# Kernel tuning notes

Measured on AMD Instinct MI355X. Metric: run time of the kernel, lower is better.

Reference implementation:

```python
import jax, jax.numpy as jnp
import numpy as np
from jax import lax

B, C, T = 8, 512, 2048
TEMP = 0.07
EPS = 1e-12


def setup_inputs() -> dict:
    key = jax.random.key(0)
    k1, k2, k3, k4 = jax.random.split(key, 4)
    x = jax.random.normal(k1, (B, C, T), dtype=jnp.float32)
    w_qkv = jax.random.normal(k2, (3 * C, C, 1), dtype=jnp.float32) * (1.0 / np.sqrt(C))
    w_dw = jax.random.normal(k3, (3 * C, 1, 3), dtype=jnp.float32) * (1.0 / np.sqrt(3))
    w_proj = jax.random.normal(k4, (C, C, 1), dtype=jnp.float32) * (1.0 / np.sqrt(C))
    return {"x": x, "w_qkv": w_qkv, "w_dw": w_dw, "w_proj": w_proj}


def _l2norm_ch(a):
    # F.normalize(a, dim=1): divide by L2 norm over channel dim, clamped at eps
    n = jnp.sqrt(jnp.sum(a * a, axis=1, keepdims=True))
    return a / jnp.maximum(n, EPS)


def reference(x, w_qkv, w_dw, w_proj):
    # 1x1 conv: [B,C,T] x [3C,C] -> [B,3C,T]
    qkv = jnp.einsum('bct,oc->bot', x, w_qkv[:, :, 0])
    # depthwise conv, kernel 3, padding 1, groups = 3C
    qkv = lax.conv_general_dilated(
        qkv, w_dw, window_strides=(1,), padding=[(1, 1)],
        dimension_numbers=('NCH', 'OIH', 'NCH'), feature_group_count=3 * C)
    q, k, v = jnp.split(qkv, 3, axis=1)  # each [B,C,T]
    q = _l2norm_ch(q)
    k = _l2norm_ch(k)
    # attn over tokens: [B,T,T]
    attn = jax.nn.softmax(jnp.einsum('bct,bcs->bts', q, k) / TEMP, axis=-1)
    out = jnp.einsum('bts,bcs->bct', attn, v)  # [B,C,T]
    return jnp.einsum('bct,oc->bot', out, w_proj[:, :, 0])
```

## Files before the change

### kernel.cpp

```cpp
#include <hip/hip_runtime.h>
#include <math.h>

static constexpr int B_ = 8, C_ = 512, T_ = 2048, C3_ = 1536;
static constexpr float INV_TEMP = 1.0f / 0.07f;

typedef __attribute__((ext_vector_type(8))) short short8;
typedef __attribute__((ext_vector_type(4))) float floatx4;

__device__ __forceinline__ float b2f(unsigned short u) {
  union { unsigned int i; float f; } v; v.i = ((unsigned int)u) << 16; return v.f;
}
__device__ __forceinline__ unsigned short f2b(float f) {
  union { float f; unsigned int i; } v; v.f = f;
  const unsigned int x = v.i;
  return (unsigned short)((x + 0x7FFFu + ((x >> 16) & 1u)) >> 16);
}
__device__ __forceinline__ void gld16(const unsigned short* g, unsigned short* l) {
  __builtin_amdgcn_global_load_lds(
      (const __attribute__((address_space(1))) void*)g,
      (__attribute__((address_space(3))) void*)l, 16, 0, 0);
}

template<int TM, bool OUT_BF16, int MODE>
__global__ __launch_bounds__(256)
void gemm_tn(const unsigned short* __restrict__ A, const unsigned short* __restrict__ B,
             void* __restrict__ Cout, int K, int lda, int ldb, int ldc,
             long long sA, long long sB, long long sC,
             const float* __restrict__ rs, const float* __restrict__ cs,
             float* __restrict__ denom, int rcStride, float scale)
{
  constexpr int NFA = TM / 64 * 2;

  const int bz = blockIdx.z;
  A += (long long)bz * sA;
  B += (long long)bz * sB;
  if (MODE == 2) { rs += (long long)bz * rcStride; cs += (long long)bz * rcStride;
                   denom += (long long)bz * rcStride; }
  if (MODE == 3) { rs += (long long)bz * rcStride; }
  const int m0 = blockIdx.y * TM, n0 = blockIdx.x * 128;
  const int tid = threadIdx.x;
  const int w = tid >> 6, lane = tid & 63;
  const int wm = (w >> 1) * (TM / 2), wn = (w & 1) * 64;
  const int rl = lane & 15, qd = lane >> 4;

  __shared__ __align__(16) unsigned short As[2][TM * 32];
  __shared__ __align__(16) unsigned short Bs[2][128 * 32];

  const int sr = lane >> 2, sg = lane & 3;
  const int aml0 = (TM == 128 ? 32 * w : 16 * w) + sr, aml1 = aml0 + 16;
  const int aq0 = sg ^ ((aml0 >> 1) & 3), aq1 = sg ^ ((aml1 >> 1) & 3);
  const unsigned short* gA0 = A + (long long)(m0 + aml0) * lda + aq0 * 8;
  const unsigned short* gA1 = A + (long long)(m0 + aml1) * lda + aq1 * 8;
  const int bml0 = 32 * w + sr, bml1 = bml0 + 16;
  const int bq0 = sg ^ ((bml0 >> 1) & 3), bq1 = sg ^ ((bml1 >> 1) & 3);
  const unsigned short* gB0 = B + (long long)(n0 + bml0) * ldb + bq0 * 8;
  const unsigned short* gB1 = B + (long long)(n0 + bml1) * ldb + bq1 * 8;

  int aoff[NFA], boff[4];
  #pragma unroll
  for (int i = 0; i < NFA; ++i) {
    const int mr = wm + i * 16 + rl;
    aoff[i] = mr * 32 + ((qd ^ ((mr >> 1) & 3)) * 8);
  }
  #pragma unroll
  for (int j = 0; j < 4; ++j) {
    const int nr = wn + j * 16 + rl;
    boff[j] = nr * 32 + ((qd ^ ((nr >> 1) & 3)) * 8);
  }

  floatx4 acc[NFA][4];
  #pragma unroll
  for (int i = 0; i < NFA; ++i)
    #pragma unroll
    for (int j = 0; j < 4; ++j) acc[i][j] = 0.0f;

  auto stage = [&](int t, int bf) {
    const int ko = t * 32;
    gld16(gA0 + ko, As[bf] + (TM == 128 ? 32 * w : 16 * w) * 32);
    if (TM == 128) gld16(gA1 + ko, As[bf] + (32 * w + 16) * 32);
    gld16(gB0 + ko, Bs[bf] + (32 * w) * 32);
    gld16(gB1 + ko, Bs[bf] + (32 * w + 16) * 32);
  };

  const int niter = K >> 5;
  stage(0, 0);
  for (int i = 0; i < niter; ++i) {
    const int buf = i & 1;
    __syncthreads();
    short8 fa[NFA], fb[4];
    #pragma unroll
    for (int ii = 0; ii < NFA; ++ii) fa[ii] = *(const short8*)(As[buf] + aoff[ii]);
    #pragma unroll
    for (int j = 0; j < 4; ++j) fb[j] = *(const short8*)(Bs[buf] + boff[j]);
    if (i + 1 < niter) stage(i + 1, buf ^ 1);
    #pragma unroll
    for (int ii = 0; ii < NFA; ++ii)
      #pragma unroll
      for (int j = 0; j < 4; ++j)
        acc[ii][j] = __builtin_amdgcn_mfma_f32_16x16x32_bf16(fa[ii], fb[j], acc[ii][j], 0, 0, 0);
  }

  #pragma unroll
  for (int i = 0; i < NFA; ++i) {
    #pragma unroll
    for (int r = 0; r < 4; ++r) {
      const int row = m0 + wm + i * 16 + qd * 4 + r;
      float rowf = 0.f;
      if (MODE == 2) rowf = rs[row] * scale;
      if (MODE == 3) rowf = 1.0f / rs[row];
      float rsum = 0.f;
      #pragma unroll
      for (int j = 0; j < 4; ++j) {
        const int col = n0 + wn + j * 16 + rl;
        float v = acc[i][j][r];
        if (MODE == 2) {
          const float s = v * rowf * cs[col];
          const unsigned short pb = f2b(__expf(s - scale));
          rsum += b2f(pb);
          ((unsigned short*)Cout)[(long long)bz * sC + (long long)row * ldc + col] = pb;
          continue;
        }
        if (MODE == 3) v *= rowf;
        const long long idx = (long long)bz * sC + (long long)row * ldc + col;
        if (OUT_BF16) ((unsigned short*)Cout)[idx] = f2b(v);
        else          ((float*)Cout)[idx] = v;
      }
      if (MODE == 2) {
        #pragma unroll
        for (int m = 1; m < 16; m <<= 1) rsum += __shfl_xor(rsum, m);
        if (rl == 0) atomicAdd(denom + row, rsum);
      }
    }
  }
}

__global__ __launch_bounds__(256)
void zero_f(float* __restrict__ p, int n)
{
  const int i = blockIdx.x * 256 + threadIdx.x;
  if (i < n) p[i] = 0.f;
}

__global__ __launch_bounds__(256)
void conv_xT(const float* __restrict__ x, unsigned short* __restrict__ xT)
{
  const int b = blockIdx.z, t0 = blockIdx.x * 32, c0 = blockIdx.y * 32;
  const int tx = threadIdx.x & 31, ty = threadIdx.x >> 5;
  __shared__ float tile[32][33];
  const float* src = x + (long long)b * C_ * T_;
  #pragma unroll
  for (int r = 0; r < 4; ++r)
    tile[ty + 8 * r][tx] = src[(long long)(c0 + ty + 8 * r) * T_ + t0 + tx];
  __syncthreads();
  unsigned short* dst = xT + (long long)b * T_ * C_;
  #pragma unroll
  for (int r = 0; r < 4; ++r)
    dst[(long long)(t0 + ty + 8 * r) * C_ + c0 + tx] = f2b(tile[tx][ty + 8 * r]);
}

__global__ __launch_bounds__(256)
void conv_bf(const float* __restrict__ in, unsigned short* __restrict__ out, int n)
{
  const int i = blockIdx.x * 256 + threadIdx.x;
  if (i < n) out[i] = f2b(in[i]);
}

__global__ __launch_bounds__(256)
void dw_v(const unsigned short* __restrict__ qkv, const float* __restrict__ wdw,
          unsigned short* __restrict__ vout)
{
  const long long idx = (long long)blockIdx.x * 256 + threadIdx.x;
  const int t = (int)(idx % T_);
  const long long rem = idx / T_;
  const int c = (int)(rem % C_), b = (int)(rem / C_);
  const unsigned short* src = qkv + ((long long)(b * C3_ + 2 * C_ + c)) * T_;
  const float* wp = wdw + (2 * C_ + c) * 3;
  const float xm = (t > 0)      ? b2f(src[t - 1]) : 0.f;
  const float x0 = b2f(src[t]);
  const float xp = (t < T_ - 1) ? b2f(src[t + 1]) : 0.f;
  vout[(long long)(b * C_ + c) * T_ + t] = f2b(fmaf(wp[0], xm, fmaf(wp[1], x0, wp[2] * xp)));
}

__global__ __launch_bounds__(256)
void dw_qk_t(const unsigned short* __restrict__ qkv, const float* __restrict__ wdw,
             unsigned short* __restrict__ qT, unsigned short* __restrict__ kT)
{
  const int bz = blockIdx.z, b = bz >> 1, p = bz & 1;
  const int t0 = blockIdx.x * 32, c0 = blockIdx.y * 32;
  const int tx = threadIdx.x & 31, ty = threadIdx.x >> 5;
  __shared__ float tin[32][34];
  __shared__ float tout[32][33];
  const int chb = b * C3_ + p * C_;
  #pragma unroll
  for (int r = 0; r < 4; ++r) {
    const int cy = ty + 8 * r;
    const unsigned short* src = qkv + (long long)(chb + c0 + cy) * T_;
    int t = t0 - 1 + tx;
    tin[cy][tx] = (t >= 0 && t < T_) ? b2f(src[t]) : 0.f;
    if (tx < 2) {
      const int t2 = t0 + 31 + tx;
      tin[cy][32 + tx] = (t2 < T_) ? b2f(src[t2]) : 0.f;
    }
  }
  __syncthreads();
  #pragma unroll
  for (int r = 0; r < 4; ++r) {
    const int cy = ty + 8 * r;
    const float* wp = wdw + (long long)(p * C_ + c0 + cy) * 3;
    tout[tx][cy] = fmaf(wp[0], tin[cy][tx], fmaf(wp[1], tin[cy][tx + 1], wp[2] * tin[cy][tx + 2]));
  }
  __syncthreads();
  unsigned short* dst = (p == 0 ? qT : kT) + (long long)b * T_ * C_;
  #pragma unroll
  for (int r = 0; r < 4; ++r)
    dst[(long long)(t0 + ty + 8 * r) * C_ + c0 + tx] = f2b(tout[ty + 8 * r][tx]);
}

__global__ __launch_bounds__(256)
void norms_k(const unsigned short* __restrict__ qT, const unsigned short* __restrict__ kT,
             float* __restrict__ inv_nq, float* __restrict__ inv_nk)
{
  const int wave = threadIdx.x >> 6, lane = threadIdx.x & 63;
  const long long row = (long long)blockIdx.x * 4 + wave;
  const unsigned short* src = (blockIdx.y == 0 ? qT : kT) + row * C_ + lane * 8;
  const uint4 u = *(const uint4*)src;
  float ss = 0.f;
  const unsigned int uu[4] = {u.x, u.y, u.z, u.w};
  #pragma unroll
  for (int i = 0; i < 4; ++i) {
    const float lo = b2f(uu[i] & 0xFFFF), hi = b2f(uu[i] >> 16);
    ss = fmaf(lo, lo, ss); ss = fmaf(hi, hi, ss);
  }
  #pragma unroll
  for (int m = 32; m; m >>= 1) ss += __shfl_xor(ss, m);
  if (lane == 0)
    (blockIdx.y == 0 ? inv_nq : inv_nk)[row] = 1.f / fmaxf(sqrtf(ss), 1e-12f);
}

extern "C" void kernel_launch(void* const* d_in, const int* in_sizes, int n_in,
                              void* d_out, int out_size, void* d_ws, size_t ws_size,
                              hipStream_t stream)
{
  const float* x      = (const float*)d_in[0];
  const float* w_qkv  = (const float*)d_in[1];
  const float* w_dw   = (const float*)d_in[2];
  const float* w_proj = (const float*)d_in[3];
  float* out = (float*)d_out;

  char* base = (char*)d_ws;
  unsigned short* xT      = (unsigned short*)base;
  unsigned short* wqkv_bf = (unsigned short*)(base + 16777216);
  unsigned short* av_t    = (unsigned short*)base;
  char* p = base + 67108864;
  unsigned short* qT = (unsigned short*)p; p += 16777216;
  unsigned short* kT = (unsigned short*)p; p += 16777216;
  unsigned short* vb = (unsigned short*)p; p += 16777216;
  unsigned short* attn   = (unsigned short*)p;
  unsigned short* qkv_bf = (unsigned short*)p;
  p += 67108864;
  unsigned short* wproj_bf = (unsigned short*)p; p += 524288;
  float* inv_nq = (float*)p; p += 65536;
  float* inv_nk = (float*)p; p += 65536;
  float* denom  = (float*)p;

  const long long TC = (long long)T_ * C_, TT = (long long)T_ * T_;

  conv_xT<<<dim3(T_ / 32, C_ / 32, B_), 256, 0, stream>>>(x, xT);
  conv_bf<<<(C3_ * C_) / 256, 256, 0, stream>>>(w_qkv, wqkv_bf, C3_ * C_);
  conv_bf<<<(C_ * C_) / 256, 256, 0, stream>>>(w_proj, wproj_bf, C_ * C_);
  zero_f<<<(B_ * T_) / 256, 256, 0, stream>>>(denom, B_ * T_);

  gemm_tn<128, true, 0><<<dim3(16, 12, B_), 256, 0, stream>>>(
      wqkv_bf, xT, qkv_bf, C_, C_, C_, T_,
      0LL, TC, (long long)C3_ * T_, nullptr, nullptr, nullptr, 0, 1.f);

  dw_v<<<(int)(((long long)B_ * C_ * T_) / 256), 256, 0, stream>>>(qkv_bf, w_dw, vb);
  dw_qk_t<<<dim3(T_ / 32, C_ / 32, B_ * 2), 256, 0, stream>>>(qkv_bf, w_dw, qT, kT);

  norms_k<<<dim3((B_ * T_) / 4, 2), 256, 0, stream>>>(qT, kT, inv_nq, inv_nk);

  gemm_tn<128, true, 2><<<dim3(16, 16, B_), 256, 0, stream>>>(
      qT, kT, attn, C_, C_, C_, T_,
      TC, TC, TT, inv_nq, inv_nk, denom, T_, INV_TEMP);

  gemm_tn<64, true, 3><<<dim3(4, 32, B_), 256, 0, stream>>>(
      attn, vb, av_t, T_, T_, T_, C_,
      TT, (long long)C_ * T_, TC, denom, nullptr, nullptr, T_, 1.f);

  gemm_tn<64, false, 0><<<dim3(16, 8, B_), 256, 0, stream>>>(
      wproj_bf, av_t, out, C_, C_, C_, T_,
      0LL, TC, (long long)C_ * T_, nullptr, nullptr, nullptr, 0, 1.f);
}
```

Baseline: 343.6 us.

## Replace direct global-to-LDS loads with register-staged double-buffered prefetch in GEMM

The GEMM main loop stops using global_load_lds and instead loads tiles into registers two iterations ahead, writes them into swizzled LDS double buffers, and syncs with an explicit lgkmcnt wait plus barrier. The aim is to hide global memory latency behind the MFMA work and to use wider per-thread 32-byte loads. The denominator zeroing moves into the norms kernel, which removes one kernel launch. The cost is higher register pressure from the staging registers, and the unrolled-by-two loop assumes an even iteration count.

```diff
diff --git a/kernel.cpp b/kernel.cpp
--- a/kernel.cpp
+++ b/kernel.cpp
@@ -15,11 +15,8 @@
   const unsigned int x = v.i;
   return (unsigned short)((x + 0x7FFFu + ((x >> 16) & 1u)) >> 16);
 }
-__device__ __forceinline__ void gld16(const unsigned short* g, unsigned short* l) {
-  __builtin_amdgcn_global_load_lds(
-      (const __attribute__((address_space(1))) void*)g,
-      (__attribute__((address_space(3))) void*)l, 16, 0, 0);
-}
+
+#define LGKM_BARRIER() asm volatile("s_waitcnt lgkmcnt(0)\n\ts_barrier" ::: "memory")
 
 template<int TM, bool OUT_BF16, int MODE>
 __global__ __launch_bounds__(256)
@@ -30,6 +27,7 @@
              float* __restrict__ denom, int rcStride, float scale)
 {
   constexpr int NFA = TM / 64 * 2;
+  constexpr int LA  = TM / 64;
 
   const int bz = blockIdx.z;
   A += (long long)bz * sA;
@@ -43,18 +41,26 @@
   const int wm = (w >> 1) * (TM / 2), wn = (w & 1) * 64;
   const int rl = lane & 15, qd = lane >> 4;
 
-  __shared__ __align__(16) unsigned short As[2][TM * 32];
-  __shared__ __align__(16) unsigned short Bs[2][128 * 32];
-
-  const int sr = lane >> 2, sg = lane & 3;
-  const int aml0 = (TM == 128 ? 32 * w : 16 * w) + sr, aml1 = aml0 + 16;
-  const int aq0 = sg ^ ((aml0 >> 1) & 3), aq1 = sg ^ ((aml1 >> 1) & 3);
-  const unsigned short* gA0 = A + (long long)(m0 + aml0) * lda + aq0 * 8;
-  const unsigned short* gA1 = A + (long long)(m0 + aml1) * lda + aq1 * 8;
-  const int bml0 = 32 * w + sr, bml1 = bml0 + 16;
-  const int bq0 = sg ^ ((bml0 >> 1) & 3), bq1 = sg ^ ((bml1 >> 1) & 3);
-  const unsigned short* gB0 = B + (long long)(n0 + bml0) * ldb + bq0 * 8;
-  const unsigned short* gB1 = B + (long long)(n0 + bml1) * ldb + bq1 * 8;
+  __shared__ __align__(16) unsigned short As[2 * TM * 32];
+  __shared__ __align__(16) unsigned short Bs[2 * 128 * 32];
+
+  int wa0, wa1;
+  const unsigned short* gA;
+  if (TM == 128) {
+    const int r = tid >> 1, sb = tid & 1, s = (r >> 1) & 3;
+    wa0 = r * 32 + ((2 * sb) ^ s) * 8;
+    wa1 = r * 32 + ((2 * sb + 1) ^ s) * 8;
+    gA = A + (long long)(m0 + r) * lda + sb * 16;
+  } else {
+    const int r = tid >> 2, g = tid & 3, s = (r >> 1) & 3;
+    wa0 = r * 32 + (g ^ s) * 8;
+    wa1 = 0;
+    gA = A + (long long)(m0 + r) * lda + g * 8;
+  }
+  const int rB = tid >> 1, sbB = tid & 1, sB2 = (rB >> 1) & 3;
+  const int wb0 = rB * 32 + ((2 * sbB) ^ sB2) * 8;
+  const int wb1 = rB * 32 + ((2 * sbB + 1) ^ sB2) * 8;
+  const unsigned short* gB = B + (long long)(n0 + rB) * ldb + sbB * 16;
 
   int aoff[NFA], boff[4];
   #pragma unroll
@@ -74,30 +80,64 @@
     #pragma unroll
     for (int j = 0; j < 4; ++j) acc[i][j] = 0.0f;
 
-  auto stage = [&](int t, int bf) {
-    const int ko = t * 32;
-    gld16(gA0 + ko, As[bf] + (TM == 128 ? 32 * w : 16 * w) * 32);
-    if (TM == 128) gld16(gA1 + ko, As[bf] + (32 * w + 16) * 32);
-    gld16(gB0 + ko, Bs[bf] + (32 * w) * 32);
-    gld16(gB1 + ko, Bs[bf] + (32 * w + 16) * 32);
+  uint4 ra0[LA], ra1[LA], rb0[2], rb1[2];
+
+  auto loadg = [&](int t, uint4* ra, uint4* rb) {
+    const long long ko = (long long)t * 32;
+    ra[0] = *(const uint4*)(gA + ko);
+    if (TM == 128) ra[1] = *(const uint4*)(gA + ko + 8);
+    rb[0] = *(const uint4*)(gB + ko);
+    rb[1] = *(const uint4*)(gB + ko + 8);
   };
-
-  const int niter = K >> 5;
-  stage(0, 0);
-  for (int i = 0; i < niter; ++i) {
-    const int buf = i & 1;
-    __syncthreads();
-    short8 fa[NFA], fb[4];
-    #pragma unroll
-    for (int ii = 0; ii < NFA; ++ii) fa[ii] = *(const short8*)(As[buf] + aoff[ii]);
-    #pragma unroll
-    for (int j = 0; j < 4; ++j) fb[j] = *(const short8*)(Bs[buf] + boff[j]);
-    if (i + 1 < niter) stage(i + 1, buf ^ 1);
-    #pragma unroll
-    for (int ii = 0; ii < NFA; ++ii)
+  auto writel = [&](const uint4* ra, const uint4* rb, int bf) {
+    unsigned short* as = As + bf * TM * 32;
+    unsigned short* bs = Bs + bf * 128 * 32;
+    *(uint4*)(as + wa0) = ra[0];
+    if (TM == 128) *(uint4*)(as + wa1) = ra[1];
+    *(uint4*)(bs + wb0) = rb[0];
+    *(uint4*)(bs + wb1) = rb[1];
+  };
+  auto readfrags = [&](int bf, short8* fa, short8* fb) {
+    const unsigned short* as = As + bf * TM * 32;
+    const unsigned short* bs = Bs + bf * 128 * 32;
+    #pragma unroll
+    for (int i = 0; i < NFA; ++i) fa[i] = *(const short8*)(as + aoff[i]);
+    #pragma unroll
+    for (int j = 0; j < 4; ++j) fb[j] = *(const short8*)(bs + boff[j]);
+  };
+  auto domfma = [&](short8* fa, short8* fb) {
+    #pragma unroll
+    for (int i = 0; i < NFA; ++i)
       #pragma unroll
       for (int j = 0; j < 4; ++j)
-        acc[ii][j] = __builtin_amdgcn_mfma_f32_16x16x32_bf16(fa[ii], fb[j], acc[ii][j], 0, 0, 0);
+        acc[i][j] = __builtin_amdgcn_mfma_f32_16x16x32_bf16(fa[i], fb[j], acc[i][j], 0, 0, 0);
+  };
+
+  const int niter = K >> 5;
+  loadg(0, ra0, rb0);
+  loadg(1, ra1, rb1);
+  writel(ra0, rb0, 0);
+  LGKM_BARRIER();
+
+  for (int i = 0; i < niter; i += 2) {
+    {
+      short8 fa[NFA], fb[4];
+      readfrags(0, fa, fb);
+      writel(ra1, rb1, 1);
+      if (i + 2 < niter) loadg(i + 2, ra0, rb0);
+      LGKM_BARRIER();
+      domfma(fa, fb);
+    }
+    {
+      short8 fa[NFA], fb[4];
+      readfrags(1, fa, fb);
+      if (i + 2 < niter) {
+        writel(ra0, rb0, 0);
+        if (i + 3 < niter) loadg(i + 3, ra1, rb1);
+        LGKM_BARRIER();
+      }
+      domfma(fa, fb);
+    }
   }
 
   #pragma unroll
@@ -135,13 +175,6 @@
 }
 
 __global__ __launch_bounds__(256)
-void zero_f(float* __restrict__ p, int n)
-{
-  const int i = blockIdx.x * 256 + threadIdx.x;
-  if (i < n) p[i] = 0.f;
-}
-
-__global__ __launch_bounds__(256)
 void conv_xT(const float* __restrict__ x, unsigned short* __restrict__ xT)
 {
   const int b = blockIdx.z, t0 = blockIdx.x * 32, c0 = blockIdx.y * 32;
@@ -218,7 +251,8 @@
 
 __global__ __launch_bounds__(256)
 void norms_k(const unsigned short* __restrict__ qT, const unsigned short* __restrict__ kT,
-             float* __restrict__ inv_nq, float* __restrict__ inv_nk)
+             float* __restrict__ inv_nq, float* __restrict__ inv_nk,
+             float* __restrict__ denom)
 {
   const int wave = threadIdx.x >> 6, lane = threadIdx.x & 63;
   const long long row = (long long)blockIdx.x * 4 + wave;
@@ -233,8 +267,10 @@
   }
   #pragma unroll
   for (int m = 32; m; m >>= 1) ss += __shfl_xor(ss, m);
-  if (lane == 0)
+  if (lane == 0) {
     (blockIdx.y == 0 ? inv_nq : inv_nk)[row] = 1.f / fmaxf(sqrtf(ss), 1e-12f);
+    if (blockIdx.y == 0) denom[row] = 0.f;
+  }
 }
 
 extern "C" void kernel_launch(void* const* d_in, const int* in_sizes, int n_in,
@@ -268,7 +304,6 @@
   conv_xT<<<dim3(T_ / 32, C_ / 32, B_), 256, 0, stream>>>(x, xT);
   conv_bf<<<(C3_ * C_) / 256, 256, 0, stream>>>(w_qkv, wqkv_bf, C3_ * C_);
   conv_bf<<<(C_ * C_) / 256, 256, 0, stream>>>(w_proj, wproj_bf, C_ * C_);
-  zero_f<<<(B_ * T_) / 256, 256, 0, stream>>>(denom, B_ * T_);
 
   gemm_tn<128, true, 0><<<dim3(16, 12, B_), 256, 0, stream>>>(
       wqkv_bf, xT, qkv_bf, C_, C_, C_, T_,
@@ -277,7 +312,7 @@
   dw_v<<<(int)(((long long)B_ * C_ * T_) / 256), 256, 0, stream>>>(qkv_bf, w_dw, vb);
   dw_qk_t<<<dim3(T_ / 32, C_ / 32, B_ * 2), 256, 0, stream>>>(qkv_bf, w_dw, qT, kT);
 
-  norms_k<<<dim3((B_ * T_) / 4, 2), 256, 0, stream>>>(qT, kT, inv_nq, inv_nk);
+  norms_k<<<dim3((B_ * T_) / 4, 2), 256, 0, stream>>>(qT, kT, inv_nq, inv_nk, denom);
 
   gemm_tn<128, true, 2><<<dim3(16, 16, B_), 256, 0, stream>>>(
       qT, kT, attn, C_, C_, C_, T_,
```

Result: slower. 664.5 us (+93.4%).
